# Kernel optimization log

Hardware: AMD Instinct MI355X
Metric: run time of the kernel (lower is better)

## Reference

```python
import jax, jax.numpy as jnp
import numpy as np
import math

# ---- static config (matches init_kwargs) ----
MUL = 16                       # multiplicity of 0e and 1o irreps in/out
IN_DIM = 4 * MUL               # 16x0e + 16x1o -> 16 + 48 = 64 channels
DIAMETER = 7.0
RADIUS = DIAMETER / 2.0
NRB = 8                        # num_radial_basis
STEPS = (1.0, 1.0, 1.0)
N_PATHS = 5                    # 0x0->0, 1x1->0, 0x1->1, 1x0->1, 1x1->1
WEIGHT_NUMEL = N_PATHS * MUL * MUL  # 1280


def _lattice():
    axes = []
    for st in STEPS:
        s = math.floor(RADIUS / st)
        axes.append(np.arange(-s, s + 1.0) * st)
    return np.stack(np.meshgrid(*axes, indexing='ij'), axis=-1).astype(np.float32)  # [kx,ky,kz,3]


def _radial_emb(r):
    # e3nn soft_one_hot_linspace, basis='smooth_finite', cutoff=True
    values = np.linspace(0.0, RADIUS, NRB + 2)[1:-1].astype(np.float32)
    step = values[1] - values[0]
    diff = (r[..., None] - values) / step
    def u(t):  # soft unit step: exp(-1/t) for t>0 else 0
        return np.where(t > 0.0, np.exp(-1.0 / np.where(t > 0.0, t, 1.0)), 0.0)
    return (1.14136 * math.e ** 2 * u(diff + 1.0) * u(1.0 - diff)).astype(np.float32)


def _spherical_harmonics(lat):
    # normalize=True, normalization='component': Y0 = 1, Y1 = sqrt(3) * unit_vec
    n = np.linalg.norm(lat, axis=-1, keepdims=True)
    unit = np.where(n > 0, lat / np.where(n > 0, n, 1.0), 0.0)
    return np.ones(lat.shape[:-1], np.float32), (math.sqrt(3.0) * unit).astype(np.float32)


_LAT = _lattice()
_EMB = jnp.asarray(_radial_emb(np.linalg.norm(_LAT, axis=-1)))  # [kx,ky,kz,NRB]
_sh0_np, _sh1_np = _spherical_harmonics(_LAT)
_SH0, _SH1 = jnp.asarray(_sh0_np), jnp.asarray(_sh1_np)
_eps_np = np.zeros((3, 3, 3), np.float32)
for _i, _j, _k in [(0, 1, 2), (1, 2, 0), (2, 0, 1)]:
    _eps_np[_i, _j, _k] = 1.0
    _eps_np[_i, _k, _j] = -1.0
_EPS = jnp.asarray(_eps_np)


def _build_kernel(tp_weight):
    """Radial-basis matmul + CG tensor-product -> conv kernel [out,in,kx,ky,kz]."""
    kx, ky, kz = _LAT.shape[:3]
    nk = kx * ky * kz
    w = jnp.einsum('xyzb,bn->xyzn', _EMB, tp_weight) / nk
    w = w.reshape(kx, ky, kz, N_PATHS, MUL, MUL)
    w1, w2, w3, w4, w5 = [w[..., p, :, :] for p in range(N_PATHS)]
    # e3nn path weights ('component' norm, 'element' path norm): sqrt(dim_out / fan_in)
    a0 = math.sqrt(1.0 / (2 * MUL))  # -> 0e: paths 1,2 each mul1*mul2 = MUL
    a1 = math.sqrt(3.0 / (3 * MUL))  # -> 1o: paths 3,4,5
    c1 = a0                          # w3j(0,0,0) = 1
    c2 = a0 / math.sqrt(3.0)         # w3j(1,1,0) = delta/sqrt(3)
    c3 = a1 / math.sqrt(3.0)         # w3j(0,1,1) = delta/sqrt(3)
    c4 = a1 / math.sqrt(3.0)         # w3j(1,0,1) = delta/sqrt(3)
    c5 = a1 / math.sqrt(6.0)         # w3j(1,1,1) = eps/sqrt(6)
    Kss = c1 * _SH0[..., None, None] * w1                                  # [k,u,o]
    Kvs = c2 * jnp.einsum('xyzi,xyzuo->xyzuio', _SH1, w2)                  # [k,u,3,o]
    Ksv = c3 * jnp.einsum('xyzk,xyzuo->xyzuok', _SH1, w3)                  # [k,u,o,3]
    eye3 = jnp.eye(3, dtype=w.dtype)
    Kvv = (c4 * jnp.einsum('xyz,ik,xyzuo->xyzuiok', _SH0, eye3, w4)
           + c5 * jnp.einsum('ijk,xyzj,xyzuo->xyzuiok', _EPS, _SH1, w5))   # [k,u,3,o,3]
    top = jnp.concatenate([Kss, Ksv.reshape(kx, ky, kz, MUL, 3 * MUL)], axis=-1)
    bot = jnp.concatenate([Kvs.reshape(kx, ky, kz, 3 * MUL, MUL),
                           Kvv.reshape(kx, ky, kz, 3 * MUL, 3 * MUL)], axis=-1)
    K = jnp.concatenate([top, bot], axis=-2)                               # [kx,ky,kz,in,out]
    return jnp.transpose(K, (4, 3, 0, 1, 2))                               # oixyz


def setup_inputs() -> dict:
    key = jax.random.key(0)
    k1, k2, k3, k4 = jax.random.split(key, 4)
    x = jax.random.normal(k1, (2, IN_DIM, 40, 40, 40), jnp.float32)
    sc_w0 = jax.random.normal(k2, (MUL, MUL), jnp.float32)
    sc_w1 = jax.random.normal(k3, (MUL, MUL), jnp.float32)
    tp_weight = jax.random.normal(k4, (NRB, WEIGHT_NUMEL), jnp.float32)
    return {"x": x, "sc_w0": sc_w0, "sc_w1": sc_w1, "tp_weight": tp_weight}


def reference(x, sc_w0, sc_w1, tp_weight):
    B = x.shape[0]
    sp = x.shape[2:]
    inv = 1.0 / math.sqrt(MUL)  # e3nn Linear fan-in normalization
    x0 = x[:, :MUL]                                  # [B,MUL,D,H,W]
    x1 = x[:, MUL:].reshape(B, MUL, 3, *sp)          # [B,MUL,3,D,H,W]
    sc0 = jnp.einsum('uo,budhw->bodhw', sc_w0, x0) * inv
    sc1 = jnp.einsum('uo,buidhw->boidhw', sc_w1, x1) * inv
    sc = jnp.concatenate([sc0, sc1.reshape(B, 3 * MUL, *sp)], axis=1)
    K = _build_kernel(tp_weight)
    pad = [(s // 2, s // 2) for s in K.shape[2:]]
    conv = jax.lax.conv_general_dilated(
        x, K, window_strides=(1, 1, 1), padding=pad,
        dimension_numbers=('NCDHW', 'OIDHW', 'NCDHW'))
    return sc + conv
```

## Files before the change

### kernel.cpp

```cpp
#include <hip/hip_runtime.h>
#include <stdint.h>


#define NT_REAL 179
#define NT_PAD  180
#define NGRP    45

#define XCH  1557376
#define XCHB ((size_t)XCH * 2)

typedef short s16x8 __attribute__((ext_vector_type(8)));
typedef float f32x4 __attribute__((ext_vector_type(4)));

struct Taps {
  int n;
  short dl16[NT_PAD];
  unsigned char dz[NT_PAD], dy[NT_PAD], dx[NT_PAD];
};
constexpr Taps mk_taps() {
  Taps t{};
  t.n = 0;
  for (int a = 0; a < 7; ++a)
    for (int b = 0; b < 7; ++b)
      for (int c = 0; c < 7; ++c) {
        int d2 = (a-3)*(a-3) + (b-3)*(b-3) + (c-3)*(c-3);
        if (d2 <= 12) {
          t.dz[t.n] = (unsigned char)a; t.dy[t.n] = (unsigned char)b;
          t.dx[t.n] = (unsigned char)c;
          t.dl16[t.n] = (short)((a*14 + b)*16 + c);
          ++t.n;
        }
      }
  for (int i = t.n; i < NT_PAD; ++i) {
    t.dz[i] = 3; t.dy[i] = 3; t.dx[i] = 3; t.dl16[i] = t.dl16[0];
  }
  return t;
}
__device__ constexpr Taps TAPS = mk_taps();
static_assert(mk_taps().n == NT_REAL, "tap count");

struct DL4s { unsigned long long v[NGRP]; };
constexpr DL4s mk_dl4() {
  DL4s d{};
  Taps t = mk_taps();
  for (int g = 0; g < NGRP; ++g) {
    unsigned long long v = 0;
    for (int q = 0; q < 4; ++q)
      v |= (unsigned long long)(unsigned short)t.dl16[g * 4 + q] << (16 * q);
    d.v[g] = v;
  }
  return d;
}
__device__ constexpr DL4s DL4 = mk_dl4();

static __device__ inline unsigned short f2bf(float f) {
  unsigned int u = __float_as_uint(f);
  unsigned int r = u + 0x7FFFu + ((u >> 16) & 1u);
  return (unsigned short)(r >> 16);
}

__device__ __forceinline__ void gl_lds16(const void* g, void* s) {
  __builtin_amdgcn_global_load_lds(
      (const __attribute__((address_space(1))) void*)g,
      (__attribute__((address_space(3))) void*)s, 16, 0, 0);
}

__global__ void prep(const float* __restrict__ x, const float* __restrict__ scw0,
                     const float* __restrict__ scw1, const float* __restrict__ tpw,
                     unsigned short* __restrict__ Xp, unsigned short* __restrict__ Bwp) {
  __shared__ float buf[160 * 65];
  int tid = threadIdx.x;

  if (blockIdx.x < 800) {
    int blk = blockIdx.x;
    int ys = blk % 10; int t2 = blk / 10; int iz = t2 % 40; int b = t2 / 40;
    int y0 = ys * 4;
    const float* src = x + (size_t)b * 4096000 + (size_t)iz * 1600 + (size_t)y0 * 40;
    for (int e = tid; e < 64 * 160; e += 256) {
      int ch = e / 160, i = e - ch * 160;
      buf[i * 65 + ch] = src[(size_t)ch * 64000 + i];
    }
    __syncthreads();
    for (int f = tid; f < 160 * 8; f += 256) {
      int i = f >> 3, g = f & 7;
      int yy = i / 40, xx = i - yy * 40;
      s16x8 v;
      #pragma unroll
      for (int j = 0; j < 8; ++j) v[j] = (short)f2bf(buf[i * 65 + g * 8 + j]);
      size_t pos = ((size_t)((b * 46 + iz + 3) * 46 + (y0 + yy + 3)) * 46 + (xx + 3));
      *reinterpret_cast<s16x8*>(Xp + (size_t)g * XCH + pos * 8) = v;
    }
    return;
  }

  int t = blockIdx.x - 800;
  float (*wsm)[16][16] = reinterpret_cast<float (*)[16][16]>(buf);

  int dz = TAPS.dz[t], dy = TAPS.dy[t], dx = TAPS.dx[t];
  float fz = dz - 3.0f, fy = dy - 3.0f, fx = dx - 3.0f;
  float d2 = fz*fz + fy*fy + fx*fx;
  float r = sqrtf(d2);

  const float step = 3.5f / 9.0f;
  const float Cc = 1.14136f * 7.38905609893065f;
  float emb[8];
  for (int bb = 0; bb < 8; ++bb) {
    float diff = (r - step * (bb + 1)) / step;
    float t1 = diff + 1.0f, t2 = 1.0f - diff;
    float u1 = (t1 > 0.0f) ? expf(-1.0f / t1) : 0.0f;
    float u2 = (t2 > 0.0f) ? expf(-1.0f / t2) : 0.0f;
    emb[bb] = Cc * u1 * u2;
  }

  int u = tid >> 4, o = tid & 15;
  for (int p = 0; p < 5; ++p) {
    float acc = 0.0f;
    int nidx = (p * 16 + u) * 16 + o;
    for (int bb = 0; bb < 8; ++bb) acc += emb[bb] * tpw[bb * 1280 + nidx];
    wsm[p][u][o] = acc * (1.0f / 343.0f);
  }
  __syncthreads();

  float invr = (d2 > 0.0f) ? (1.7320508075688772f / r) : 0.0f;
  float sh[3] = { fz * invr, fy * invr, fx * invr };

  bool center = (dz == 3 && dy == 3 && dx == 3);
  bool padt = (t >= NT_REAL);
  const float c1 = 0.17677669529663687f;
  const float c2 = 0.10206207261596575f;
  const float c3 = 0.14433756729740643f;
  const float c4 = 0.14433756729740643f;
  const float c5 = 0.10206207261596575f;
  const float inv = 0.25f;

  for (int e = tid; e < 4096; e += 256) {
    int ich = e & 63, och = e >> 6;
    float v = 0.0f;
    if (!padt) {
      if (och < 16) {
        if (ich < 16) {
          v = c1 * wsm[0][ich][och];
          if (center) v += inv * scw0[ich * 16 + och];
        } else {
          int qq = ich - 16; int uu = qq / 3, ii = qq % 3;
          v = c2 * sh[ii] * wsm[1][uu][och];
        }
      } else {
        int qo = och - 16; int oo = qo / 3, kk = qo % 3;
        if (ich < 16) {
          v = c3 * sh[kk] * wsm[2][ich][oo];
        } else {
          int qi = ich - 16; int uu = qi / 3, ii = qi % 3;
          if (ii == kk) {
            v = c4 * wsm[3][uu][oo];
            if (center) v += inv * scw1[uu * 16 + oo];
          } else {
            int jj = 3 - ii - kk;
            float sgn = (((kk - ii + 3) % 3) == 2) ? 1.0f : -1.0f;
            v = c5 * sgn * sh[jj] * wsm[4][uu][oo];
          }
        }
      }
    }
    int chunk = ich >> 3, j = ich & 7, q = t & 3, grp = t >> 2;
    int nt = och >> 4, n = och & 15;
    size_t idx = (((((size_t)chunk * NGRP + grp) * 4 + nt) * 4 + q) * 16 + n) * 8 + j;
    Bwp[idx] = f2bf(v);
  }
}

__global__ __launch_bounds__(256, 2) void conv3d(
    const unsigned short* __restrict__ Xp,
    const unsigned short* __restrict__ Bwp,
    float* __restrict__ out) {
  __shared__ __align__(16) unsigned char smem[71680];

  int blk = blockIdx.x;
  int p = ((blk & 7) << 6) | (blk >> 3);
  if (p >= 500) return;
  int b = p / 250; int rem = p - b * 250;
  int tz = rem / 25, ty = (rem / 5) % 5, tx = rem % 5;

  int tid = threadIdx.x;
  int lane = tid & 63;
  int w = tid >> 6;
  int q = lane >> 4, n = lane & 15;
  int qs = q << 4;

  size_t hbase = (size_t)(((b * 46 + tz * 4) * 46 + ty * 8) * 46 + tx * 8) * 16;

  int abase = w * 224 + ((n >> 3) << 4) + (n & 7);

  f32x4 acc[4][4];
  #pragma unroll
  for (int a = 0; a < 4; ++a)
    #pragma unroll
    for (int nt = 0; nt < 4; ++nt) acc[a][nt] = f32x4{0.f, 0.f, 0.f, 0.f};

  auto stageH1 = [&](int c, unsigned char* dst, int k) {
    const unsigned char* xc = (const unsigned char*)Xp + (size_t)c * XCHB + hbase;
    int sl = (k << 6) + lane;
    int hx = sl & 15; hx = hx > 13 ? 13 : hx;
    int r = sl >> 4;
    int hz = (r * 2341) >> 15;
    int hy = r - hz * 14;
    gl_lds16(xc + ((size_t)((hz * 46 + hy) * 46 + hx)) * 16, dst + (k << 10));
  };

  for (int k = w; k < 35; k += 4) stageH1(0, smem, k);
  __syncthreads();

  for (int c = 0; c < 8; ++c) {
    const unsigned char* XHc = smem + (c & 1) * 35840;
    unsigned char* XHn = smem + ((c + 1) & 1) * 35840;

    const unsigned char* bgc = (const unsigned char*)Bwp
        + (size_t)c * (NGRP * 4096) + (size_t)lane * 16;

    s16x8 bf0[4], bf1[4], bf2[4];
    auto loadB = [&](s16x8* dst, int g) {
      const s16x8* pp = (const s16x8*)(bgc + (size_t)g * 4096);
      dst[0] = pp[0]; dst[1] = pp[64]; dst[2] = pp[128]; dst[3] = pp[192];
    };
    auto compute = [&](int g, const s16x8* bfr) {
      unsigned long long dlv = DL4.v[g];
      int dl = (int)((dlv >> qs) & 0xFFFFull);
      const unsigned char* ab = XHc + ((size_t)(abase + dl) << 4);
      s16x8 a0 = *(const s16x8*)(ab);
      s16x8 a1 = *(const s16x8*)(ab + 512);
      s16x8 a2 = *(const s16x8*)(ab + 1024);
      s16x8 a3 = *(const s16x8*)(ab + 1536);
      acc[0][0] = __builtin_amdgcn_mfma_f32_16x16x32_bf16(a0, bfr[0], acc[0][0], 0, 0, 0);
      acc[0][1] = __builtin_amdgcn_mfma_f32_16x16x32_bf16(a0, bfr[1], acc[0][1], 0, 0, 0);
      acc[0][2] = __builtin_amdgcn_mfma_f32_16x16x32_bf16(a0, bfr[2], acc[0][2], 0, 0, 0);
      acc[0][3] = __builtin_amdgcn_mfma_f32_16x16x32_bf16(a0, bfr[3], acc[0][3], 0, 0, 0);
      acc[1][0] = __builtin_amdgcn_mfma_f32_16x16x32_bf16(a1, bfr[0], acc[1][0], 0, 0, 0);
      acc[1][1] = __builtin_amdgcn_mfma_f32_16x16x32_bf16(a1, bfr[1], acc[1][1], 0, 0, 0);
      acc[1][2] = __builtin_amdgcn_mfma_f32_16x16x32_bf16(a1, bfr[2], acc[1][2], 0, 0, 0);
      acc[1][3] = __builtin_amdgcn_mfma_f32_16x16x32_bf16(a1, bfr[3], acc[1][3], 0, 0, 0);
      acc[2][0] = __builtin_amdgcn_mfma_f32_16x16x32_bf16(a2, bfr[0], acc[2][0], 0, 0, 0);
      acc[2][1] = __builtin_amdgcn_mfma_f32_16x16x32_bf16(a2, bfr[1], acc[2][1], 0, 0, 0);
      acc[2][2] = __builtin_amdgcn_mfma_f32_16x16x32_bf16(a2, bfr[2], acc[2][2], 0, 0, 0);
      acc[2][3] = __builtin_amdgcn_mfma_f32_16x16x32_bf16(a2, bfr[3], acc[2][3], 0, 0, 0);
      acc[3][0] = __builtin_amdgcn_mfma_f32_16x16x32_bf16(a3, bfr[0], acc[3][0], 0, 0, 0);
      acc[3][1] = __builtin_amdgcn_mfma_f32_16x16x32_bf16(a3, bfr[1], acc[3][1], 0, 0, 0);
      acc[3][2] = __builtin_amdgcn_mfma_f32_16x16x32_bf16(a3, bfr[2], acc[3][2], 0, 0, 0);
      acc[3][3] = __builtin_amdgcn_mfma_f32_16x16x32_bf16(a3, bfr[3], acc[3][3], 0, 0, 0);
    };

    loadB(bf0, 0);
    loadB(bf1, 1);
    #pragma unroll 1
    for (int g = 0; g < NGRP; g += 3) {
      if (c < 7 && g >= 12 && g <= 36) {
        int k = ((g - 12) / 3) * 4 + w;
        if (k < 35) stageH1(c + 1, XHn, k);
      }
      int g2 = g + 2 < NGRP ? g + 2 : NGRP - 1;
      int g3 = g + 3 < NGRP ? g + 3 : NGRP - 1;
      int g4 = g + 4 < NGRP ? g + 4 : NGRP - 1;
      loadB(bf2, g2);
      compute(g, bf0);
      loadB(bf0, g3);
      compute(g + 1, bf1);
      loadB(bf1, g4);
      compute(g + 2, bf2);
    }
    __syncthreads();
  }

  #pragma unroll
  for (int nt = 0; nt < 4; ++nt) {
    size_t cb = (size_t)(b * 64 + nt * 16 + n) * 64000
              + (size_t)(tz * 4 + w) * 1600
              + (size_t)(tx * 8 + (q & 1) * 4);
    #pragma unroll
    for (int a = 0; a < 4; ++a) {
      float* dst = out + cb + (size_t)(ty * 8 + a * 2 + (q >> 1)) * 40;
      *reinterpret_cast<f32x4*>(dst) = acc[a][nt];
    }
  }
}

extern "C" void kernel_launch(void* const* d_in, const int* in_sizes, int n_in,
                              void* d_out, int out_size, void* d_ws, size_t ws_size,
                              hipStream_t stream) {
  const float* x    = (const float*)d_in[0];
  const float* scw0 = (const float*)d_in[1];
  const float* scw1 = (const float*)d_in[2];
  const float* tpw  = (const float*)d_in[3];
  float* out = (float*)d_out;

  unsigned short* Xp  = (unsigned short*)d_ws;
  unsigned short* Bwp = Xp + (size_t)8 * XCH;

  hipMemsetAsync(Xp, 0, (size_t)8 * XCH * 2, stream);
  prep<<<800 + NT_PAD, 256, 0, stream>>>(x, scw0, scw1, tpw, Xp, Bwp);
  conv3d<<<512, 256, 0, stream>>>(Xp, Bwp, out);
}
```

Before: 243.3 us.

## Fuse padding zero-fill into prep and software-pipeline A/B fragment loads

The prep kernel now covers every padded 46x46 row, one block per row, and writes zeros for halo positions itself. This removes the separate hipMemsetAsync over the padded input buffer. In the conv kernel, the A fragments from LDS are now loaded one group ahead into rotating registers alongside the B fragments, and next-channel staging is spread one slice per group across waves. The extra live registers may lower occupancy, and the prep grid grows to many small blocks.

```diff
diff --git a/kernel.cpp b/kernel.cpp
--- a/kernel.cpp
+++ b/kernel.cpp
@@ -68,32 +68,41 @@
 __global__ void prep(const float* __restrict__ x, const float* __restrict__ scw0,
                      const float* __restrict__ scw1, const float* __restrict__ tpw,
                      unsigned short* __restrict__ Xp, unsigned short* __restrict__ Bwp) {
-  __shared__ float buf[160 * 65];
+  __shared__ float buf[40 * 65];
   int tid = threadIdx.x;
 
-  if (blockIdx.x < 800) {
+  if (blockIdx.x < 4232) {
     int blk = blockIdx.x;
-    int ys = blk % 10; int t2 = blk / 10; int iz = t2 % 40; int b = t2 / 40;
-    int y0 = ys * 4;
-    const float* src = x + (size_t)b * 4096000 + (size_t)iz * 1600 + (size_t)y0 * 40;
-    for (int e = tid; e < 64 * 160; e += 256) {
-      int ch = e / 160, i = e - ch * 160;
-      buf[i * 65 + ch] = src[(size_t)ch * 64000 + i];
+    int yp = blk % 46; int t2 = blk / 46; int zp = t2 % 46; int b = t2 / 46;
+    int iz = zp - 3, iy = yp - 3;
+    bool rowin = ((unsigned)iz < 40u) && ((unsigned)iy < 40u);
+    if (rowin) {
+      const float* src = x + (size_t)b * 4096000 + (size_t)iz * 1600 + (size_t)iy * 40;
+      for (int e = tid; e < 64 * 40; e += 256) {
+        int ch = e >> 5; int h = e & 31;
+        (void)h;
+      }
+      for (int e = tid; e < 64 * 40; e += 256) {
+        int ch = e / 40, xx = e - ch * 40;
+        buf[xx * 65 + ch] = src[(size_t)ch * 64000 + xx];
+      }
     }
     __syncthreads();
-    for (int f = tid; f < 160 * 8; f += 256) {
-      int i = f >> 3, g = f & 7;
-      int yy = i / 40, xx = i - yy * 40;
-      s16x8 v;
-      #pragma unroll
-      for (int j = 0; j < 8; ++j) v[j] = (short)f2bf(buf[i * 65 + g * 8 + j]);
-      size_t pos = ((size_t)((b * 46 + iz + 3) * 46 + (y0 + yy + 3)) * 46 + (xx + 3));
+    for (int f = tid; f < 46 * 8; f += 256) {
+      int xp = f >> 3, g = f & 7;
+      s16x8 v = s16x8{0, 0, 0, 0, 0, 0, 0, 0};
+      int ix = xp - 3;
+      if (rowin && (unsigned)ix < 40u) {
+        #pragma unroll
+        for (int j = 0; j < 8; ++j) v[j] = (short)f2bf(buf[ix * 65 + g * 8 + j]);
+      }
+      size_t pos = (size_t)blk * 46 + xp;
       *reinterpret_cast<s16x8*>(Xp + (size_t)g * XCH + pos * 8) = v;
     }
     return;
   }
 
-  int t = blockIdx.x - 800;
+  int t = blockIdx.x - 4232;
   float (*wsm)[16][16] = reinterpret_cast<float (*)[16][16]>(buf);
 
   int dz = TAPS.dz[t], dy = TAPS.dy[t], dx = TAPS.dx[t];
@@ -210,6 +219,8 @@
   for (int k = w; k < 35; k += 4) stageH1(0, smem, k);
   __syncthreads();
 
+  s16x8 A0[4], A1[4], A2[4], B0[4], B1[4], B2[4];
+
   for (int c = 0; c < 8; ++c) {
     const unsigned char* XHc = smem + (c & 1) * 35840;
     unsigned char* XHn = smem + ((c + 1) & 1) * 35840;
@@ -217,54 +228,58 @@
     const unsigned char* bgc = (const unsigned char*)Bwp
         + (size_t)c * (NGRP * 4096) + (size_t)lane * 16;
 
-    s16x8 bf0[4], bf1[4], bf2[4];
     auto loadB = [&](s16x8* dst, int g) {
       const s16x8* pp = (const s16x8*)(bgc + (size_t)g * 4096);
       dst[0] = pp[0]; dst[1] = pp[64]; dst[2] = pp[128]; dst[3] = pp[192];
     };
-    auto compute = [&](int g, const s16x8* bfr) {
+    auto loadA = [&](s16x8* dst, int g) {
       unsigned long long dlv = DL4.v[g];
       int dl = (int)((dlv >> qs) & 0xFFFFull);
       const unsigned char* ab = XHc + ((size_t)(abase + dl) << 4);
-      s16x8 a0 = *(const s16x8*)(ab);
-      s16x8 a1 = *(const s16x8*)(ab + 512);
-      s16x8 a2 = *(const s16x8*)(ab + 1024);
-      s16x8 a3 = *(const s16x8*)(ab + 1536);
-      acc[0][0] = __builtin_amdgcn_mfma_f32_16x16x32_bf16(a0, bfr[0], acc[0][0], 0, 0, 0);
-      acc[0][1] = __builtin_amdgcn_mfma_f32_16x16x32_bf16(a0, bfr[1], acc[0][1], 0, 0, 0);
-      acc[0][2] = __builtin_amdgcn_mfma_f32_16x16x32_bf16(a0, bfr[2], acc[0][2], 0, 0, 0);
-      acc[0][3] = __builtin_amdgcn_mfma_f32_16x16x32_bf16(a0, bfr[3], acc[0][3], 0, 0, 0);
-      acc[1][0] = __builtin_amdgcn_mfma_f32_16x16x32_bf16(a1, bfr[0], acc[1][0], 0, 0, 0);
-      acc[1][1] = __builtin_amdgcn_mfma_f32_16x16x32_bf16(a1, bfr[1], acc[1][1], 0, 0, 0);
-      acc[1][2] = __builtin_amdgcn_mfma_f32_16x16x32_bf16(a1, bfr[2], acc[1][2], 0, 0, 0);
-      acc[1][3] = __builtin_amdgcn_mfma_f32_16x16x32_bf16(a1, bfr[3], acc[1][3], 0, 0, 0);
-      acc[2][0] = __builtin_amdgcn_mfma_f32_16x16x32_bf16(a2, bfr[0], acc[2][0], 0, 0, 0);
-      acc[2][1] = __builtin_amdgcn_mfma_f32_16x16x32_bf16(a2, bfr[1], acc[2][1], 0, 0, 0);
-      acc[2][2] = __builtin_amdgcn_mfma_f32_16x16x32_bf16(a2, bfr[2], acc[2][2], 0, 0, 0);
-      acc[2][3] = __builtin_amdgcn_mfma_f32_16x16x32_bf16(a2, bfr[3], acc[2][3], 0, 0, 0);
-      acc[3][0] = __builtin_amdgcn_mfma_f32_16x16x32_bf16(a3, bfr[0], acc[3][0], 0, 0, 0);
-      acc[3][1] = __builtin_amdgcn_mfma_f32_16x16x32_bf16(a3, bfr[1], acc[3][1], 0, 0, 0);
-      acc[3][2] = __builtin_amdgcn_mfma_f32_16x16x32_bf16(a3, bfr[2], acc[3][2], 0, 0, 0);
-      acc[3][3] = __builtin_amdgcn_mfma_f32_16x16x32_bf16(a3, bfr[3], acc[3][3], 0, 0, 0);
+      dst[0] = *(const s16x8*)(ab);
+      dst[1] = *(const s16x8*)(ab + 512);
+      dst[2] = *(const s16x8*)(ab + 1024);
+      dst[3] = *(const s16x8*)(ab + 1536);
     };
-
-    loadB(bf0, 0);
-    loadB(bf1, 1);
+    auto computeG = [&](const s16x8* A, const s16x8* B) {
+      acc[0][0] = __builtin_amdgcn_mfma_f32_16x16x32_bf16(A[0], B[0], acc[0][0], 0, 0, 0);
+      acc[0][1] = __builtin_amdgcn_mfma_f32_16x16x32_bf16(A[0], B[1], acc[0][1], 0, 0, 0);
+      acc[0][2] = __builtin_amdgcn_mfma_f32_16x16x32_bf16(A[0], B[2], acc[0][2], 0, 0, 0);
+      acc[0][3] = __builtin_amdgcn_mfma_f32_16x16x32_bf16(A[0], B[3], acc[0][3], 0, 0, 0);
+      acc[1][0] = __builtin_amdgcn_mfma_f32_16x16x32_bf16(A[1], B[0], acc[1][0], 0, 0, 0);
+      acc[1][1] = __builtin_amdgcn_mfma_f32_16x16x32_bf16(A[1], B[1], acc[1][1], 0, 0, 0);
+      acc[1][2] = __builtin_amdgcn_mfma_f32_16x16x32_bf16(A[1], B[2], acc[1][2], 0, 0, 0);
+      acc[1][3] = __builtin_amdgcn_mfma_f32_16x16x32_bf16(A[1], B[3], acc[1][3], 0, 0, 0);
+      acc[2][0] = __builtin_amdgcn_mfma_f32_16x16x32_bf16(A[2], B[0], acc[2][0], 0, 0, 0);
+      acc[2][1] = __builtin_amdgcn_mfma_f32_16x16x32_bf16(A[2], B[1], acc[2][1], 0, 0, 0);
+      acc[2][2] = __builtin_amdgcn_mfma_f32_16x16x32_bf16(A[2], B[2], acc[2][2], 0, 0, 0);
+      acc[2][3] = __builtin_amdgcn_mfma_f32_16x16x32_bf16(A[2], B[3], acc[2][3], 0, 0, 0);
+      acc[3][0] = __builtin_amdgcn_mfma_f32_16x16x32_bf16(A[3], B[0], acc[3][0], 0, 0, 0);
+      acc[3][1] = __builtin_amdgcn_mfma_f32_16x16x32_bf16(A[3], B[1], acc[3][1], 0, 0, 0);
+      acc[3][2] = __builtin_amdgcn_mfma_f32_16x16x32_bf16(A[3], B[2], acc[3][2], 0, 0, 0);
+      acc[3][3] = __builtin_amdgcn_mfma_f32_16x16x32_bf16(A[3], B[3], acc[3][3], 0, 0, 0);
+    };
+
+    loadA(A0, 0); loadB(B0, 0);
+    loadA(A1, 1); loadB(B1, 1);
+    loadA(A2, 2); loadB(B2, 2);
+
     #pragma unroll 1
     for (int g = 0; g < NGRP; g += 3) {
-      if (c < 7 && g >= 12 && g <= 36) {
-        int k = ((g - 12) / 3) * 4 + w;
-        if (k < 35) stageH1(c + 1, XHn, k);
-      }
-      int g2 = g + 2 < NGRP ? g + 2 : NGRP - 1;
-      int g3 = g + 3 < NGRP ? g + 3 : NGRP - 1;
-      int g4 = g + 4 < NGRP ? g + 4 : NGRP - 1;
-      loadB(bf2, g2);
-      compute(g, bf0);
-      loadB(bf0, g3);
-      compute(g + 1, bf1);
-      loadB(bf1, g4);
-      compute(g + 2, bf2);
+      if (c < 7 && g >= 8 && g < 43 && w == ((g - 8) & 3))
+        stageH1(c + 1, XHn, g - 8);
+      computeG(A0, B0);
+      if (g + 3 < NGRP) { loadA(A0, g + 3); loadB(B0, g + 3); }
+
+      if (c < 7 && g + 1 >= 8 && g + 1 < 43 && w == ((g - 7) & 3))
+        stageH1(c + 1, XHn, g - 7);
+      computeG(A1, B1);
+      if (g + 4 < NGRP) { loadA(A1, g + 4); loadB(B1, g + 4); }
+
+      if (c < 7 && g + 2 >= 8 && g + 2 < 43 && w == ((g - 6) & 3))
+        stageH1(c + 1, XHn, g - 6);
+      computeG(A2, B2);
+      if (g + 5 < NGRP) { loadA(A2, g + 5); loadB(B2, g + 5); }
     }
     __syncthreads();
   }
@@ -294,7 +309,6 @@
   unsigned short* Xp  = (unsigned short*)d_ws;
   unsigned short* Bwp = Xp + (size_t)8 * XCH;
 
-  hipMemsetAsync(Xp, 0, (size_t)8 * XCH * 2, stream);
-  prep<<<800 + NT_PAD, 256, 0, stream>>>(x, scw0, scw1, tpw, Xp, Bwp);
+  prep<<<4232 + NT_PAD, 256, 0, stream>>>(x, scw0, scw1, tpw, Xp, Bwp);
   conv3d<<<512, 256, 0, stream>>>(Xp, Bwp, out);
 }
```

Measured after the change: 236.4 us. 2.8% less time.
